# Optimization experiments

Hardware: AMD Instinct MI355X
Metric: run time of the kernel (lower is better)

The kernel has to match this reference:

```python
import jax, jax.numpy as jnp
import numpy as np


def _gcn_layer(x, W, b, src, dst, norm, n_nodes):
    # x: [N, Fin]; transform first (PyG GCNConv): h = x @ W
    h = x @ W  # [N, Fout]
    # gather-scale-scatter: out[d] += norm_e * h[s] over edges (incl. self loops)
    msgs = h[src] * norm[:, None]  # [E+N, Fout]
    agg = jax.ops.segment_sum(msgs, dst, num_segments=n_nodes)
    return agg + b


def setup_inputs() -> dict:
    key = jax.random.key(0)
    k1, k2, k3, k4 = jax.random.split(key, 4)
    N, E, F_IN, HID, OUT = 50000, 800000, 128, 256, 128
    x = jax.random.normal(k1, (N, F_IN), dtype=jnp.float32)
    edge_index = jax.random.randint(k2, (2, E), 0, N, dtype=jnp.int64)
    W1 = jax.random.normal(k3, (F_IN, HID), dtype=jnp.float32) / np.sqrt(F_IN)
    b1 = jnp.zeros((HID,), dtype=jnp.float32)
    W2 = jax.random.normal(k4, (HID, OUT), dtype=jnp.float32) / np.sqrt(HID)
    b2 = jnp.zeros((OUT,), dtype=jnp.float32)
    return {"x": x, "edge_index": edge_index, "W1": W1, "b1": b1, "W2": W2, "b2": b2}


def reference(x, edge_index, W1, b1, W2, b2):
    N = x.shape[0]
    # GCN normalization with self loops: A_hat = D^-1/2 (A + I) D^-1/2
    self_loops = jnp.arange(N, dtype=edge_index.dtype)
    src = jnp.concatenate([edge_index[0], self_loops])
    dst = jnp.concatenate([edge_index[1], self_loops])
    deg = jax.ops.segment_sum(jnp.ones_like(dst, dtype=x.dtype), dst, num_segments=N)
    dinv = jnp.where(deg > 0, jax.lax.rsqrt(deg), 0.0)
    norm = dinv[src] * dinv[dst]  # [E+N]
    h = _gcn_layer(x, W1, b1, src, dst, norm, N)
    h = jax.nn.relu(h)  # dropout is identity in eval mode
    out = _gcn_layer(h, W2, b2, src, dst, norm, N)
    return out  # unsupervised mode returns raw embeddings [N, 128]
```

## Files before the change

kernel.cpp:

```cpp
#include <hip/hip_runtime.h>
#include <hip/hip_bf16.h>


static constexpr int N_NODES = 50000;
static constexpr int N_EDGES = 800000;
static constexpr int F_IN = 128;
static constexpr int HID  = 256;
static constexpr int F_OUT = 128;
static constexpr int H2P  = 258;
static constexpr int NREP = 16;

typedef __attribute__((ext_vector_type(8))) short short8;
typedef __attribute__((ext_vector_type(4))) float f32x4;

__device__ __forceinline__ unsigned short f2bf(float f) {
    union { float f; unsigned u; } x; x.f = f;
    unsigned r = x.u + 0x7FFF + ((x.u >> 16) & 1);
    return (unsigned short)(r >> 16);
}
__device__ __forceinline__ float bf2f(unsigned short h) {
    union { unsigned u; float f; } x; x.u = ((unsigned)h) << 16;
    return x.f;
}

__global__ void deg_wt_kernel(const int* __restrict__ dst, int* __restrict__ deg,
                              int* __restrict__ pos, int E,
                              const float* __restrict__ W1, unsigned short* __restrict__ w1t,
                              const float* __restrict__ W2, unsigned short* __restrict__ w2t,
                              int EB, int NB1) {
    const int b = blockIdx.x;
    if (b < EB) {
        int i = b * 256 + threadIdx.x;
        if (i < E) pos[i] = atomicAdd(&deg[dst[i]], 1);
    } else if (b < EB + NB1) {
        int t = (b - EB) * 256 + threadIdx.x;
        if (t < F_IN * HID) {
            int n = t / F_IN, k = t - n * F_IN;
            unsigned short v = f2bf(W1[(size_t)k * HID + n]);
#pragma unroll
            for (int r = 0; r < NREP; r++) w1t[(size_t)r * F_IN * HID + t] = v;
        }
    } else {
        int t = (b - EB - NB1) * 256 + threadIdx.x;
        if (t < HID * F_OUT) {
            int n = t / HID, k = t - n * HID;
            unsigned short v = f2bf(W2[(size_t)k * F_OUT + n]);
#pragma unroll
            for (int r = 0; r < NREP; r++) w2t[(size_t)r * HID * F_OUT + t] = v;
        }
    }
}

__global__ __launch_bounds__(256) void scan_reduce_dinv(const int* __restrict__ deg,
                                                        int* __restrict__ bsums,
                                                        float* __restrict__ dinv, int N) {
    int i = blockIdx.x * 256 + threadIdx.x;
    int v = (i < N) ? deg[i] : 0;
    if (i < N) dinv[i] = rsqrtf((float)(v + 1));
#pragma unroll
    for (int ofs = 32; ofs > 0; ofs >>= 1) v += __shfl_down(v, ofs);
    __shared__ int ws[4];
    if ((threadIdx.x & 63) == 0) ws[threadIdx.x >> 6] = v;
    __syncthreads();
    if (threadIdx.x == 0) bsums[blockIdx.x] = ws[0] + ws[1] + ws[2] + ws[3];
}

__global__ __launch_bounds__(256) void scan_final_scalex(const int* __restrict__ deg,
                                                         const int* __restrict__ bsums,
                                                         int* __restrict__ off, int N, int nb,
                                                         const float* __restrict__ x,
                                                         const float* __restrict__ dinv,
                                                         unsigned short* __restrict__ xs) {
    const int tid = threadIdx.x;
    if ((int)blockIdx.x >= nb) {
        int i = (blockIdx.x - nb) * 256 + tid;
        if (i < N_NODES * F_IN / 8) {
            float dv = dinv[i >> 4];
            float4 v0 = ((const float4*)x)[i * 2];
            float4 v1 = ((const float4*)x)[i * 2 + 1];
            short8 o;
            o[0] = (short)f2bf(v0.x * dv); o[1] = (short)f2bf(v0.y * dv);
            o[2] = (short)f2bf(v0.z * dv); o[3] = (short)f2bf(v0.w * dv);
            o[4] = (short)f2bf(v1.x * dv); o[5] = (short)f2bf(v1.y * dv);
            o[6] = (short)f2bf(v1.z * dv); o[7] = (short)f2bf(v1.w * dv);
            *(short8*)(xs + (size_t)i * 8) = o;
        }
        return;
    }
    __shared__ int bs[256];
    __shared__ int s[256];
    bs[tid] = (tid < nb) ? bsums[tid] : 0;
    const int i = blockIdx.x * 256 + tid;
    int v = (i < N) ? deg[i] : 0;
    s[tid] = v;
    __syncthreads();
    for (int ofs = 1; ofs < 256; ofs <<= 1) {
        int tb = (tid >= ofs) ? bs[tid - ofs] : 0;
        int tv = (tid >= ofs) ? s[tid - ofs] : 0;
        __syncthreads();
        bs[tid] += tb;
        s[tid] += tv;
        __syncthreads();
    }
    int bbase = (blockIdx.x == 0) ? 0 : bs[blockIdx.x - 1];
    int excl = (tid == 0) ? 0 : s[tid - 1];
    if (i <= N) off[i] = bbase + excl;
}

__global__ void scatter_kernel(const int* __restrict__ src, const int* __restrict__ dst,
                               const int* __restrict__ pos, const int* __restrict__ off,
                               int* __restrict__ csr, int E) {
    int i = blockIdx.x * blockDim.x + threadIdx.x;
    if (i < E) csr[off[dst[i]] + pos[i]] = src[i];
}

template <int MODE>
__global__ __launch_bounds__(256) void agg_bf16(const unsigned short* __restrict__ hs,
                                                const int* __restrict__ off,
                                                const int* __restrict__ csr,
                                                const float* __restrict__ dinv,
                                                const float* __restrict__ bias,
                                                void* __restrict__ outp, int N) {
    const int wid = threadIdx.x >> 6;
    const int n = blockIdx.x * 4 + wid;
    if (n >= N) return;
    const int lane = threadIdx.x & 63;
    const int lane16 = lane & 15;
    const int slot = lane >> 4;

    float va[8], vb[8], vc[8], vd[8];
#pragma unroll
    for (int j = 0; j < 8; j++) { va[j] = 0.f; vb[j] = 0.f; vc[j] = 0.f; vd[j] = 0.f; }

    if (slot == 0) {
        short8 s = *(const short8*)(hs + (size_t)n * 128 + lane16 * 8);
#pragma unroll
        for (int j = 0; j < 8; j++) va[j] = bf2f((unsigned short)s[j]);
    }

    const int e0 = off[n];
    const int e1 = off[n + 1];
    for (int e = e0 + slot; e < e1; e += 16) {
        const int i1 = e + 4, i2 = e + 8, i3 = e + 12;
        const float f1 = (i1 < e1) ? 1.f : 0.f;
        const float f2 = (i2 < e1) ? 1.f : 0.f;
        const float f3 = (i3 < e1) ? 1.f : 0.f;
        const int c1 = min(i1, e1 - 1), c2 = min(i2, e1 - 1), c3 = min(i3, e1 - 1);
        int s0 = csr[e];
        int s1 = csr[c1];
        int s2 = csr[c2];
        int s3 = csr[c3];
        short8 v0 = *(const short8*)(hs + (size_t)s0 * 128 + lane16 * 8);
        short8 v1 = *(const short8*)(hs + (size_t)s1 * 128 + lane16 * 8);
        short8 v2 = *(const short8*)(hs + (size_t)s2 * 128 + lane16 * 8);
        short8 v3 = *(const short8*)(hs + (size_t)s3 * 128 + lane16 * 8);
#pragma unroll
        for (int j = 0; j < 8; j++) va[j] += bf2f((unsigned short)v0[j]);
#pragma unroll
        for (int j = 0; j < 8; j++) vb[j] = fmaf(f1, bf2f((unsigned short)v1[j]), vb[j]);
#pragma unroll
        for (int j = 0; j < 8; j++) vc[j] = fmaf(f2, bf2f((unsigned short)v2[j]), vc[j]);
#pragma unroll
        for (int j = 0; j < 8; j++) vd[j] = fmaf(f3, bf2f((unsigned short)v3[j]), vd[j]);
    }
#pragma unroll
    for (int j = 0; j < 8; j++) va[j] += vb[j] + vc[j] + vd[j];

#pragma unroll
    for (int j = 0; j < 8; j++) va[j] += __shfl_down(va[j], 32);
#pragma unroll
    for (int j = 0; j < 8; j++) va[j] += __shfl_down(va[j], 16);

    if (lane < 16) {
        float dv = dinv[n];
        if (MODE == 0) {
            short8 o;
#pragma unroll
            for (int j = 0; j < 8; j++) o[j] = (short)f2bf(va[j] * dv);
            *(short8*)((unsigned short*)outp + (size_t)n * 128 + lane * 8) = o;
        } else {
            float* op = (float*)outp + (size_t)n * 128 + lane * 8;
            float4 o0, o1;
            o0.x = va[0] * dv + bias[lane * 8 + 0];
            o0.y = va[1] * dv + bias[lane * 8 + 1];
            o0.z = va[2] * dv + bias[lane * 8 + 2];
            o0.w = va[3] * dv + bias[lane * 8 + 3];
            o1.x = va[4] * dv + bias[lane * 8 + 4];
            o1.y = va[5] * dv + bias[lane * 8 + 5];
            o1.z = va[6] * dv + bias[lane * 8 + 6];
            o1.w = va[7] * dv + bias[lane * 8 + 7];
            ((float4*)op)[0] = o0;
            ((float4*)op)[1] = o1;
        }
    }
}

__global__ __launch_bounds__(512, 2) void gemm12(const unsigned short* __restrict__ Y,
                                                 const unsigned short* __restrict__ w1t,
                                                 const float* __restrict__ b1,
                                                 const unsigned short* __restrict__ w2t,
                                                 const float* __restrict__ dinv,
                                                 unsigned short* __restrict__ hs2, int M) {
    __shared__ unsigned short w1l[F_IN * HID];
    __shared__ unsigned short w2l[HID * F_OUT];
    __shared__ unsigned short h2s[16 * H2P];

    const int tid = threadIdx.x;
    const int wid = tid >> 6;
    const int lane = tid & 63;
    const int an = lane & 15;
    const int q = lane >> 4;
    const int rep = blockIdx.x & (NREP - 1);

    {
        const unsigned short* w1r = w1t + (size_t)rep * F_IN * HID;
        const unsigned short* w2r = w2t + (size_t)rep * HID * F_OUT;
        for (int i = tid; i < 4096; i += 512) {
            const int cw = i >> 9;
            const int t  = (i >> 8) & 1;
            const int c  = (i >> 6) & 3;
            const int l  = i & 63;
            const int col = cw * 32 + t * 16 + (l & 15);
            const int off = col * F_IN + (l >> 4) * 8 + c * 32;
            *(short8*)(w1l + (size_t)i * 8) = *(const short8*)(w1r + off);
        }
        for (int i = tid; i < 4096; i += 512) {
            const int cw = i >> 9;
            const int c  = (i >> 6) & 7;
            const int l  = i & 63;
            const int colB = cw * 16 + (l & 15);
            const int off = colB * HID + (l >> 4) * 8 + c * 32;
            *(short8*)(w2l + (size_t)i * 8) = *(const short8*)(w2r + off);
        }
    }
    float bv0 = b1[wid * 32 + an];
    float bv1 = b1[wid * 32 + 16 + an];
    __syncthreads();

    const int T = M >> 4;
    for (int t0 = blockIdx.x; t0 < T; t0 += gridDim.x) {
        const int m0 = t0 * 16;

        short8 a[4];
        {
            const unsigned short* yp = Y + (size_t)(m0 + an) * F_IN + q * 8;
#pragma unroll
            for (int c = 0; c < 4; c++) a[c] = *(const short8*)(yp + c * 32);
        }
        f32x4 accA0 = {0.f, 0.f, 0.f, 0.f};
        f32x4 accA1 = {0.f, 0.f, 0.f, 0.f};
#pragma unroll
        for (int c = 0; c < 4; c++) {
            const short8 b0 = *(const short8*)(w1l + ((size_t)((wid * 8 + c) * 64 + lane)) * 8);
            const short8 b1f = *(const short8*)(w1l + ((size_t)((wid * 8 + 4 + c) * 64 + lane)) * 8);
            accA0 = __builtin_amdgcn_mfma_f32_16x16x32_bf16(a[c], b0, accA0, 0, 0, 0);
            accA1 = __builtin_amdgcn_mfma_f32_16x16x32_bf16(a[c], b1f, accA1, 0, 0, 0);
        }
        {
            const int c0 = wid * 32 + an;
            unsigned short* hrow = &h2s[(q * 4) * H2P];
#pragma unroll
            for (int rr = 0; rr < 4; rr++) {
                hrow[rr * H2P + c0]      = f2bf(fmaxf(accA0[rr] + bv0, 0.f));
                hrow[rr * H2P + c0 + 16] = f2bf(fmaxf(accA1[rr] + bv1, 0.f));
            }
        }
        __syncthreads();

        {
            short8 h[8];
            const unsigned short* hp = &h2s[an * H2P + q * 8];
#pragma unroll
            for (int c = 0; c < 8; c++) h[c] = *(const short8*)(hp + c * 32);
            f32x4 acc = {0.f, 0.f, 0.f, 0.f};
#pragma unroll
            for (int c = 0; c < 8; c++) {
                const short8 b2f = *(const short8*)(w2l + ((size_t)((wid * 8 + c) * 64 + lane)) * 8);
                acc = __builtin_amdgcn_mfma_f32_16x16x32_bf16(h[c], b2f, acc, 0, 0, 0);
            }
            const float4 dv4 = ((const float4*)dinv)[(m0 >> 2) + q];
            unsigned short* op = hs2 + (size_t)(m0 + q * 4) * F_OUT + wid * 16 + an;
            op[0]         = f2bf(acc[0] * dv4.x);
            op[F_OUT]     = f2bf(acc[1] * dv4.y);
            op[2 * F_OUT] = f2bf(acc[2] * dv4.z);
            op[3 * F_OUT] = f2bf(acc[3] * dv4.w);
        }
        __syncthreads();
    }
}

extern "C" void kernel_launch(void* const* d_in, const int* in_sizes, int n_in,
                              void* d_out, int out_size, void* d_ws, size_t ws_size,
                              hipStream_t stream) {
    const float* x  = (const float*)d_in[0];
    const int*   ei = (const int*)d_in[1];
    const float* W1 = (const float*)d_in[2];
    const float* b1 = (const float*)d_in[3];
    const float* W2 = (const float*)d_in[4];
    const float* b2 = (const float*)d_in[5];

    const int N = N_NODES;
    const int E = N_EDGES;
    const int* srcp = ei;
    const int* dstp = ei + E;

    char* base = (char*)d_ws;
    size_t o = 0;
    auto alloc = [&](size_t bytes) {
        void* p = base + o;
        o = (o + bytes + 255) & ~(size_t)255;
        return p;
    };
    int*            deg  = (int*)alloc((size_t)N * 4);
    int*            offs = (int*)alloc((size_t)(N + 1) * 4);
    float*          dinv = (float*)alloc((size_t)N * 4);
    int*            bsum = (int*)alloc(256 * 4);
    int*            pos  = (int*)alloc((size_t)E * 4);
    int*            csr  = (int*)alloc((size_t)E * 4);
    unsigned short* xs   = (unsigned short*)alloc((size_t)N * F_IN * 2);
    unsigned short* Y    = (unsigned short*)alloc((size_t)N * F_IN * 2);
    unsigned short* w1t  = (unsigned short*)alloc((size_t)NREP * F_IN * HID * 2);
    unsigned short* w2t  = (unsigned short*)alloc((size_t)NREP * HID * F_OUT * 2);
    unsigned short* hs2  = xs;

    hipMemsetAsync(deg, 0, (size_t)N * 4, stream);

    const int NB  = (N + 256) / 256;
    const int NBX = (N * F_IN / 8 + 255) / 256;
    const int EB  = (E + 255) / 256;
    const int NB1 = (F_IN * HID + 255) / 256;
    const int NB2 = (HID * F_OUT + 255) / 256;

    deg_wt_kernel<<<EB + NB1 + NB2, 256, 0, stream>>>(dstp, deg, pos, E, W1, w1t, W2, w2t, EB, NB1);
    scan_reduce_dinv<<<NB, 256, 0, stream>>>(deg, bsum, dinv, N);
    scan_final_scalex<<<NB + NBX, 256, 0, stream>>>(deg, bsum, offs, N, NB, x, dinv, xs);
    scatter_kernel<<<EB, 256, 0, stream>>>(srcp, dstp, pos, offs, csr, E);

    agg_bf16<0><<<(N + 3) / 4, 256, 0, stream>>>(xs, offs, csr, dinv, nullptr, Y, N);
    gemm12<<<256, 512, 0, stream>>>(Y, w1t, b1, w2t, dinv, hs2, N);
    agg_bf16<1><<<(N + 3) / 4, 256, 0, stream>>>(hs2, offs, csr, dinv, b2, d_out, N);
}
```

Measured before the change: 260.6 us.

## Process 64-row tiles in fused GEMM with XOR-swizzled shared hidden buffer

The fused two-layer transform kernel now handles 64 rows per iteration instead of 16. Each weight fragment read from LDS is reused across four row sub-tiles, and there are a quarter as many barriers per row. The padded hidden buffer is replaced by a larger 64x256 buffer with an XOR swizzle to avoid LDS bank conflicts. The larger LDS footprint and extra registers may lower occupancy under the two-blocks-per-CU launch bound, and a ragged last tile needs bounds checks.

```diff
diff --git a/kernel.cpp b/kernel.cpp
--- a/kernel.cpp
+++ b/kernel.cpp
@@ -7,7 +7,6 @@
 static constexpr int F_IN = 128;
 static constexpr int HID  = 256;
 static constexpr int F_OUT = 128;
-static constexpr int H2P  = 258;
 static constexpr int NREP = 16;
 
 typedef __attribute__((ext_vector_type(8))) short short8;
@@ -203,7 +202,7 @@
                                                  unsigned short* __restrict__ hs2, int M) {
     __shared__ unsigned short w1l[F_IN * HID];
     __shared__ unsigned short w2l[HID * F_OUT];
-    __shared__ unsigned short h2s[16 * H2P];
+    __shared__ unsigned short h2s[64 * 256];
 
     const int tid = threadIdx.x;
     const int wid = tid >> 6;
@@ -233,57 +232,77 @@
             *(short8*)(w2l + (size_t)i * 8) = *(const short8*)(w2r + off);
         }
     }
-    float bv0 = b1[wid * 32 + an];
-    float bv1 = b1[wid * 32 + 16 + an];
+    const float bv0 = b1[wid * 32 + an];
+    const float bv1 = b1[wid * 32 + 16 + an];
     __syncthreads();
 
-    const int T = M >> 4;
+    const int T = (M + 63) >> 6;
     for (int t0 = blockIdx.x; t0 < T; t0 += gridDim.x) {
-        const int m0 = t0 * 16;
-
-        short8 a[4];
-        {
-            const unsigned short* yp = Y + (size_t)(m0 + an) * F_IN + q * 8;
-#pragma unroll
-            for (int c = 0; c < 4; c++) a[c] = *(const short8*)(yp + c * 32);
-        }
-        f32x4 accA0 = {0.f, 0.f, 0.f, 0.f};
-        f32x4 accA1 = {0.f, 0.f, 0.f, 0.f};
+        const int m0 = t0 * 64;
+
+        short8 a[4][4];
+#pragma unroll
+        for (int s = 0; s < 4; s++) {
+            int row = m0 + s * 16 + an;
+            if (row >= M) row = M - 1;
+            const unsigned short* yp = Y + (size_t)row * F_IN + q * 8;
+#pragma unroll
+            for (int c = 0; c < 4; c++) a[s][c] = *(const short8*)(yp + c * 32);
+        }
+        f32x4 acc[4][2];
+#pragma unroll
+        for (int s = 0; s < 4; s++) {
+            acc[s][0] = (f32x4){0.f, 0.f, 0.f, 0.f};
+            acc[s][1] = (f32x4){0.f, 0.f, 0.f, 0.f};
+        }
 #pragma unroll
         for (int c = 0; c < 4; c++) {
             const short8 b0 = *(const short8*)(w1l + ((size_t)((wid * 8 + c) * 64 + lane)) * 8);
             const short8 b1f = *(const short8*)(w1l + ((size_t)((wid * 8 + 4 + c) * 64 + lane)) * 8);
-            accA0 = __builtin_amdgcn_mfma_f32_16x16x32_bf16(a[c], b0, accA0, 0, 0, 0);
-            accA1 = __builtin_amdgcn_mfma_f32_16x16x32_bf16(a[c], b1f, accA1, 0, 0, 0);
+#pragma unroll
+            for (int s = 0; s < 4; s++) {
+                acc[s][0] = __builtin_amdgcn_mfma_f32_16x16x32_bf16(a[s][c], b0, acc[s][0], 0, 0, 0);
+                acc[s][1] = __builtin_amdgcn_mfma_f32_16x16x32_bf16(a[s][c], b1f, acc[s][1], 0, 0, 0);
+            }
         }
         {
             const int c0 = wid * 32 + an;
-            unsigned short* hrow = &h2s[(q * 4) * H2P];
+#pragma unroll
+            for (int s = 0; s < 4; s++) {
+#pragma unroll
+                for (int rr = 0; rr < 4; rr++) {
+                    const int brow = s * 16 + q * 4 + rr;
+                    const int base = brow * 256;
+                    const int xr = (brow & 7) << 4;
+                    *(unsigned short*)((char*)h2s + (((base + c0) * 2) ^ xr)) =
+                        f2bf(fmaxf(acc[s][0][rr] + bv0, 0.f));
+                    *(unsigned short*)((char*)h2s + (((base + c0 + 16) * 2) ^ xr)) =
+                        f2bf(fmaxf(acc[s][1][rr] + bv1, 0.f));
+                }
+            }
+        }
+        __syncthreads();
+
+#pragma unroll
+        for (int s = 0; s < 4; s++) {
+            const int rbase = s * 16 + an;
+            const int xr = (rbase & 7) << 4;
+            f32x4 accB = {0.f, 0.f, 0.f, 0.f};
+#pragma unroll
+            for (int c = 0; c < 8; c++) {
+                const short8 h = *(const short8*)((const char*)h2s +
+                                  (((rbase * 256 + c * 32 + q * 8) * 2) ^ xr));
+                const short8 b2f = *(const short8*)(w2l + ((size_t)((wid * 8 + c) * 64 + lane)) * 8);
+                accB = __builtin_amdgcn_mfma_f32_16x16x32_bf16(h, b2f, accB, 0, 0, 0);
+            }
+            const int mbase = m0 + s * 16;
+            const float4 dv4 = ((const float4*)dinv)[(mbase >> 2) + q];
+            unsigned short* op = hs2 + (size_t)(mbase + q * 4) * F_OUT + wid * 16 + an;
+            const float dvs[4] = {dv4.x, dv4.y, dv4.z, dv4.w};
 #pragma unroll
             for (int rr = 0; rr < 4; rr++) {
-                hrow[rr * H2P + c0]      = f2bf(fmaxf(accA0[rr] + bv0, 0.f));
-                hrow[rr * H2P + c0 + 16] = f2bf(fmaxf(accA1[rr] + bv1, 0.f));
+                if (mbase + q * 4 + rr < M) op[rr * F_OUT] = f2bf(accB[rr] * dvs[rr]);
             }
-        }
-        __syncthreads();
-
-        {
-            short8 h[8];
-            const unsigned short* hp = &h2s[an * H2P + q * 8];
-#pragma unroll
-            for (int c = 0; c < 8; c++) h[c] = *(const short8*)(hp + c * 32);
-            f32x4 acc = {0.f, 0.f, 0.f, 0.f};
-#pragma unroll
-            for (int c = 0; c < 8; c++) {
-                const short8 b2f = *(const short8*)(w2l + ((size_t)((wid * 8 + c) * 64 + lane)) * 8);
-                acc = __builtin_amdgcn_mfma_f32_16x16x32_bf16(h[c], b2f, acc, 0, 0, 0);
-            }
-            const float4 dv4 = ((const float4*)dinv)[(m0 >> 2) + q];
-            unsigned short* op = hs2 + (size_t)(m0 + q * 4) * F_OUT + wid * 16 + an;
-            op[0]         = f2bf(acc[0] * dv4.x);
-            op[F_OUT]     = f2bf(acc[1] * dv4.y);
-            op[2 * F_OUT] = f2bf(acc[2] * dv4.z);
-            op[3 * F_OUT] = f2bf(acc[3] * dv4.w);
         }
         __syncthreads();
     }
```

After: 247.7 us. 1.05x faster.

## Split fused two-layer GEMM into separate kernels with per-wave row tiles

Applied to the files above, without the earlier changes.

Replaces the fused gemm12 kernel, which kept the hidden activations in shared memory and needed block-wide syncs between the two matmuls, with two kernels. Each wave now owns 16 rows and computes every output column, with one block per 128 rows instead of a persistent 256-block grid. The hidden layer is written to a new global bf16 buffer of N×256 and read back by the second kernel. This removes the __syncthreads barriers and halves the shared memory each kernel needs, which may raise occupancy. The cost is an extra global round trip of about 25 MB, an extra launch, and each block reloading the weight tiles into shared memory, with many more blocks than before.

```diff
diff --git a/kernel.cpp b/kernel.cpp
--- a/kernel.cpp
+++ b/kernel.cpp
@@ -7,7 +7,6 @@
 static constexpr int F_IN = 128;
 static constexpr int HID  = 256;
 static constexpr int F_OUT = 128;
-static constexpr int H2P  = 258;
 static constexpr int NREP = 16;
 
 typedef __attribute__((ext_vector_type(8))) short short8;
@@ -195,15 +194,11 @@
     }
 }
 
-__global__ __launch_bounds__(512, 2) void gemm12(const unsigned short* __restrict__ Y,
-                                                 const unsigned short* __restrict__ w1t,
-                                                 const float* __restrict__ b1,
-                                                 const unsigned short* __restrict__ w2t,
-                                                 const float* __restrict__ dinv,
-                                                 unsigned short* __restrict__ hs2, int M) {
+__global__ __launch_bounds__(512, 2) void gemm1(const unsigned short* __restrict__ Y,
+                                                const unsigned short* __restrict__ w1t,
+                                                const float* __restrict__ b1,
+                                                unsigned short* __restrict__ h2, int M) {
     __shared__ unsigned short w1l[F_IN * HID];
-    __shared__ unsigned short w2l[HID * F_OUT];
-    __shared__ unsigned short h2s[16 * H2P];
 
     const int tid = threadIdx.x;
     const int wid = tid >> 6;
@@ -214,7 +209,6 @@
 
     {
         const unsigned short* w1r = w1t + (size_t)rep * F_IN * HID;
-        const unsigned short* w2r = w2t + (size_t)rep * HID * F_OUT;
         for (int i = tid; i < 4096; i += 512) {
             const int cw = i >> 9;
             const int t  = (i >> 8) & 1;
@@ -224,6 +218,55 @@
             const int off = col * F_IN + (l >> 4) * 8 + c * 32;
             *(short8*)(w1l + (size_t)i * 8) = *(const short8*)(w1r + off);
         }
+    }
+    float bvs[16];
+#pragma unroll
+    for (int t = 0; t < 16; t++) bvs[t] = b1[t * 16 + an];
+    __syncthreads();
+
+    const int m0 = blockIdx.x * 128 + wid * 16;
+    int row = m0 + an;
+    if (row >= M) row = M - 1;
+    short8 a[4];
+    {
+        const unsigned short* yp = Y + (size_t)row * F_IN + q * 8;
+#pragma unroll
+        for (int c = 0; c < 4; c++) a[c] = *(const short8*)(yp + c * 32);
+    }
+    const int mb = m0 + q * 4;
+#pragma unroll
+    for (int tt = 0; tt < 16; tt++) {
+        f32x4 acc = {0.f, 0.f, 0.f, 0.f};
+#pragma unroll
+        for (int c = 0; c < 4; c++) {
+            const short8 b = *(const short8*)(w1l +
+                              ((size_t)(((tt >> 1) * 8 + (tt & 1) * 4 + c) * 64 + lane)) * 8);
+            acc = __builtin_amdgcn_mfma_f32_16x16x32_bf16(a[c], b, acc, 0, 0, 0);
+        }
+        const int col = tt * 16 + an;
+#pragma unroll
+        for (int rr = 0; rr < 4; rr++) {
+            const int m = mb + rr;
+            if (m < M) h2[(size_t)m * HID + col] = f2bf(fmaxf(acc[rr] + bvs[tt], 0.f));
+        }
+    }
+}
+
+__global__ __launch_bounds__(512, 2) void gemm2(const unsigned short* __restrict__ h2,
+                                                const unsigned short* __restrict__ w2t,
+                                                const float* __restrict__ dinv,
+                                                unsigned short* __restrict__ hs2, int M) {
+    __shared__ unsigned short w2l[HID * F_OUT];
+
+    const int tid = threadIdx.x;
+    const int wid = tid >> 6;
+    const int lane = tid & 63;
+    const int an = lane & 15;
+    const int q = lane >> 4;
+    const int rep = blockIdx.x & (NREP - 1);
+
+    {
+        const unsigned short* w2r = w2t + (size_t)rep * HID * F_OUT;
         for (int i = tid; i < 4096; i += 512) {
             const int cw = i >> 9;
             const int c  = (i >> 6) & 7;
@@ -233,59 +276,35 @@
             *(short8*)(w2l + (size_t)i * 8) = *(const short8*)(w2r + off);
         }
     }
-    float bv0 = b1[wid * 32 + an];
-    float bv1 = b1[wid * 32 + 16 + an];
     __syncthreads();
 
-    const int T = M >> 4;
-    for (int t0 = blockIdx.x; t0 < T; t0 += gridDim.x) {
-        const int m0 = t0 * 16;
-
-        short8 a[4];
-        {
-            const unsigned short* yp = Y + (size_t)(m0 + an) * F_IN + q * 8;
-#pragma unroll
-            for (int c = 0; c < 4; c++) a[c] = *(const short8*)(yp + c * 32);
-        }
-        f32x4 accA0 = {0.f, 0.f, 0.f, 0.f};
-        f32x4 accA1 = {0.f, 0.f, 0.f, 0.f};
-#pragma unroll
-        for (int c = 0; c < 4; c++) {
-            const short8 b0 = *(const short8*)(w1l + ((size_t)((wid * 8 + c) * 64 + lane)) * 8);
-            const short8 b1f = *(const short8*)(w1l + ((size_t)((wid * 8 + 4 + c) * 64 + lane)) * 8);
-            accA0 = __builtin_amdgcn_mfma_f32_16x16x32_bf16(a[c], b0, accA0, 0, 0, 0);
-            accA1 = __builtin_amdgcn_mfma_f32_16x16x32_bf16(a[c], b1f, accA1, 0, 0, 0);
-        }
-        {
-            const int c0 = wid * 32 + an;
-            unsigned short* hrow = &h2s[(q * 4) * H2P];
-#pragma unroll
-            for (int rr = 0; rr < 4; rr++) {
-                hrow[rr * H2P + c0]      = f2bf(fmaxf(accA0[rr] + bv0, 0.f));
-                hrow[rr * H2P + c0 + 16] = f2bf(fmaxf(accA1[rr] + bv1, 0.f));
-            }
-        }
-        __syncthreads();
-
-        {
-            short8 h[8];
-            const unsigned short* hp = &h2s[an * H2P + q * 8];
-#pragma unroll
-            for (int c = 0; c < 8; c++) h[c] = *(const short8*)(hp + c * 32);
-            f32x4 acc = {0.f, 0.f, 0.f, 0.f};
-#pragma unroll
-            for (int c = 0; c < 8; c++) {
-                const short8 b2f = *(const short8*)(w2l + ((size_t)((wid * 8 + c) * 64 + lane)) * 8);
-                acc = __builtin_amdgcn_mfma_f32_16x16x32_bf16(h[c], b2f, acc, 0, 0, 0);
-            }
-            const float4 dv4 = ((const float4*)dinv)[(m0 >> 2) + q];
-            unsigned short* op = hs2 + (size_t)(m0 + q * 4) * F_OUT + wid * 16 + an;
-            op[0]         = f2bf(acc[0] * dv4.x);
-            op[F_OUT]     = f2bf(acc[1] * dv4.y);
-            op[2 * F_OUT] = f2bf(acc[2] * dv4.z);
-            op[3 * F_OUT] = f2bf(acc[3] * dv4.w);
-        }
-        __syncthreads();
+    const int m0 = blockIdx.x * 128 + wid * 16;
+    int row = m0 + an;
+    if (row >= M) row = M - 1;
+    short8 a[8];
+    {
+        const unsigned short* hp = h2 + (size_t)row * HID + q * 8;
+#pragma unroll
+        for (int c = 0; c < 8; c++) a[c] = *(const short8*)(hp + c * 32);
+    }
+    const int mb = m0 + q * 4;
+    float dv[4];
+#pragma unroll
+    for (int rr = 0; rr < 4; rr++) dv[rr] = (mb + rr < M) ? dinv[mb + rr] : 0.f;
+#pragma unroll
+    for (int tt = 0; tt < 8; tt++) {
+        f32x4 acc = {0.f, 0.f, 0.f, 0.f};
+#pragma unroll
+        for (int c = 0; c < 8; c++) {
+            const short8 b = *(const short8*)(w2l + ((size_t)((tt * 8 + c) * 64 + lane)) * 8);
+            acc = __builtin_amdgcn_mfma_f32_16x16x32_bf16(a[c], b, acc, 0, 0, 0);
+        }
+        const int col = tt * 16 + an;
+#pragma unroll
+        for (int rr = 0; rr < 4; rr++) {
+            const int m = mb + rr;
+            if (m < M) hs2[(size_t)m * F_OUT + col] = f2bf(acc[rr] * dv[rr]);
+        }
     }
 }
 
@@ -319,6 +338,7 @@
     int*            csr  = (int*)alloc((size_t)E * 4);
     unsigned short* xs   = (unsigned short*)alloc((size_t)N * F_IN * 2);
     unsigned short* Y    = (unsigned short*)alloc((size_t)N * F_IN * 2);
+    unsigned short* h2   = (unsigned short*)alloc((size_t)N * HID * 2);
     unsigned short* w1t  = (unsigned short*)alloc((size_t)NREP * F_IN * HID * 2);
     unsigned short* w2t  = (unsigned short*)alloc((size_t)NREP * HID * F_OUT * 2);
     unsigned short* hs2  = xs;
@@ -330,6 +350,7 @@
     const int EB  = (E + 255) / 256;
     const int NB1 = (F_IN * HID + 255) / 256;
     const int NB2 = (HID * F_OUT + 255) / 256;
+    const int GB  = (N + 127) / 128;
 
     deg_wt_kernel<<<EB + NB1 + NB2, 256, 0, stream>>>(dstp, deg, pos, E, W1, w1t, W2, w2t, EB, NB1);
     scan_reduce_dinv<<<NB, 256, 0, stream>>>(deg, bsum, dinv, N);
@@ -337,6 +358,7 @@
     scatter_kernel<<<EB, 256, 0, stream>>>(srcp, dstp, pos, offs, csr, E);
 
     agg_bf16<0><<<(N + 3) / 4, 256, 0, stream>>>(xs, offs, csr, dinv, nullptr, Y, N);
-    gemm12<<<256, 512, 0, stream>>>(Y, w1t, b1, w2t, dinv, hs2, N);
+    gemm1<<<GB, 512, 0, stream>>>(Y, w1t, b1, h2, N);
+    gemm2<<<GB, 512, 0, stream>>>(h2, w2t, dinv, hs2, N);
     agg_bf16<1><<<(N + 3) / 4, 256, 0, stream>>>(hs2, offs, csr, dinv, b2, d_out, N);
 }
```

Measured after the change: 237.5 us. -8.9%, faster.
